# Kernel optimization log

Measured on AMD Instinct MI355X. Metric: run time of the kernel, lower is better.

Reference implementation:

```python
import jax, jax.numpy as jnp
import numpy as np

ITERATION = 3
NEG = -2.0**16 + 1.0  # mask fill value from the torch code


def setup_inputs() -> dict:
    key = jax.random.key(0)
    k1, k2, k3, k4 = jax.random.split(key, 4)
    B, L, D_in, D_out, K = 1024, 512, 64, 64, 8
    low_capsule = jax.random.normal(k1, (B, L, D_in), dtype=jnp.float32)
    B_init = jax.random.normal(k2, (1, K, L), dtype=jnp.float32)
    S = jax.random.normal(k3, (D_in, D_out), dtype=jnp.float32)
    seq_len = jax.random.randint(k4, (B, 1), 1, L + 1, dtype=jnp.int32)
    return {"low_capsule": low_capsule, "B_init": B_init, "S": S, "seq_len": seq_len}


def _squash(x):
    # torch code sums squared norm over dim=1 (the capsule/max_k dim), keepdim
    sq = jnp.sum(jnp.square(x), axis=1, keepdims=True)
    scale = sq / (1.0 + sq) / jnp.sqrt(sq + 1e-9)
    return scale * x


def reference(low_capsule, B_init, S, seq_len):
    # low_capsule: [B, L, D_in], B_init: [1, K, L], S: [D_in, D_out], seq_len: [B, 1]
    Bsz, L, _ = low_capsule.shape
    K = B_init.shape[1]
    # sequence mask: [B, K, L] (seq_len tiled over K)
    mask = jnp.arange(L, dtype=seq_len.dtype)[None, None, :] < seq_len[:, :, None]
    mask = jnp.broadcast_to(mask, (Bsz, K, L))
    # bilinear projection is loop-invariant; compute once
    low_new = jnp.einsum('bld,do->blo', low_capsule, S)  # [B, L, D_out]
    B_mat = B_init
    high = None
    for _ in range(ITERATION):
        logits = jnp.where(mask, B_mat, NEG)               # [B, K, L]
        W = jax.nn.softmax(logits, axis=-1)                # masked softmax
        high = _squash(jnp.einsum('bkl,blo->bko', W, low_new))  # [B, K, D_out]
        B_delta = jnp.sum(jnp.einsum('bko,blo->bkl', high, low_new),
                          axis=0, keepdims=True)           # [1, K, L]
        B_mat = B_mat + B_delta
    return high
```

## Files before the change

kernel.cpp:

```cpp
#include <hip/hip_runtime.h>

#define NEG_FILL (-65535.0f)
#define NSLOT 32

typedef __attribute__((ext_vector_type(8))) short  short8;
typedef __attribute__((ext_vector_type(4))) float  floatx4;

__device__ inline unsigned short f2bf(float f) {
    unsigned u = __float_as_uint(f);
    u += 0x7FFFu + ((u >> 16) & 1u);
    return (unsigned short)(u >> 16);
}
__device__ inline float bf2f(unsigned short h) {
    return __uint_as_float(((unsigned)h) << 16);
}
__device__ __forceinline__ short8 pack8(float4 a, float4 b) {
    short8 f;
    f[0] = (short)f2bf(a.x); f[1] = (short)f2bf(a.y);
    f[2] = (short)f2bf(a.z); f[3] = (short)f2bf(a.w);
    f[4] = (short)f2bf(b.x); f[5] = (short)f2bf(b.y);
    f[6] = (short)f2bf(b.z); f[7] = (short)f2bf(b.w);
    return f;
}

__global__ __launch_bounds__(256) void k_init(const float* __restrict__ Binit,
                                              float* __restrict__ B0,
                                              float* __restrict__ slots) {
    int i = blockIdx.x * 256 + threadIdx.x;
    slots[i] = 0.f;
    if (i < 4096) B0[i] = Binit[i];
}

__global__ __launch_bounds__(256) void k_bred(const float* __restrict__ Bcur,
                                              float* __restrict__ Bnext,
                                              float* __restrict__ slots) {
    int i = blockIdx.x * 256 + threadIdx.x;
    float s = Bcur[i];
    #pragma unroll
    for (int j = 0; j < NSLOT; ++j) {
        s += slots[j * 4096 + i];
        slots[j * 4096 + i] = 0.f;
    }
    Bnext[i] = s;
}

__device__ __forceinline__ void softmax_to_WsT(
    const float* __restrict__ Bc, int sl, int lane, int g,
    float (*WsT)[8]) {
    #pragma unroll
    for (int kk = 0; kk < 2; ++kk) {
        const int k = g + (kk << 2);
        float v[8];
        float mx = NEG_FILL;
        #pragma unroll
        for (int j = 0; j < 8; ++j) {
            int l = lane + (j << 6);
            v[j] = (l < sl) ? Bc[(k << 9) + l] : NEG_FILL;
            mx = fmaxf(mx, v[j]);
        }
        #pragma unroll
        for (int off = 32; off; off >>= 1) mx = fmaxf(mx, __shfl_xor(mx, off));
        float s = 0.f;
        #pragma unroll
        for (int j = 0; j < 8; ++j) { v[j] = expf(v[j] - mx); s += v[j]; }
        #pragma unroll
        for (int off = 32; off; off >>= 1) s += __shfl_xor(s, off);
        const float inv = 1.0f / s;
        #pragma unroll
        for (int j = 0; j < 8; ++j) WsT[lane + (j << 6)][k] = v[j] * inv;
    }
}

__global__ __launch_bounds__(256, 4) void k_lnT(
    const float* __restrict__ low,
    const float* __restrict__ S,
    const float* __restrict__ Bc,
    const int* __restrict__ seq_len,
    unsigned short* __restrict__ ln,
    float* __restrict__ hout)
{
    __shared__ __align__(16) float WsT[512][8];
    __shared__ __align__(16) float Tpart[4][8][64];
    __shared__ __align__(16) float Tred[8][64];

    const int t = threadIdx.x, lane = t & 63, g = t >> 6, b = blockIdx.x;
    const int m = lane & 15, q = lane >> 4;
    const int sl = seq_len[b];
    const float* lowb = low + ((size_t)b << 15);
    unsigned short* lnb = ln + ((size_t)b << 15);

    softmax_to_WsT(Bc, sl, lane, g, WsT);
    __syncthreads();

    short8 sfrag[4][2];
    #pragma unroll
    for (int nt = 0; nt < 4; ++nt)
        #pragma unroll
        for (int dh = 0; dh < 2; ++dh) {
            short8 f;
            #pragma unroll
            for (int j = 0; j < 8; ++j) {
                int d = dh * 32 + q * 8 + j;
                f[j] = (short)f2bf(S[(d << 6) + nt * 16 + m]);
            }
            sfrag[nt][dh] = f;
        }

    float Tp[8][4];
    #pragma unroll
    for (int k = 0; k < 8; ++k)
        #pragma unroll
        for (int nt = 0; nt < 4; ++nt) Tp[k][nt] = 0.f;

    for (int tt = 0; tt < 8; ++tt) {
        const int lt = (g << 7) + (tt << 4);
        short8 afrag[2];
        #pragma unroll
        for (int dh = 0; dh < 2; ++dh) {
            const float4* p =
                (const float4*)&lowb[((lt + m) << 6) + dh * 32 + q * 8];
            float4 x0 = p[0], x1 = p[1];
            short8 f;
            f[0] = (short)f2bf(x0.x); f[1] = (short)f2bf(x0.y);
            f[2] = (short)f2bf(x0.z); f[3] = (short)f2bf(x0.w);
            f[4] = (short)f2bf(x1.x); f[5] = (short)f2bf(x1.y);
            f[6] = (short)f2bf(x1.z); f[7] = (short)f2bf(x1.w);
            afrag[dh] = f;
        }
        float lnr[4][4];
        #pragma unroll
        for (int nt = 0; nt < 4; ++nt) {
            floatx4 acc = {0.f, 0.f, 0.f, 0.f};
            acc = __builtin_amdgcn_mfma_f32_16x16x32_bf16(afrag[0], sfrag[nt][0], acc, 0, 0, 0);
            acc = __builtin_amdgcn_mfma_f32_16x16x32_bf16(afrag[1], sfrag[nt][1], acc, 0, 0, 0);
            #pragma unroll
            for (int r = 0; r < 4; ++r) {
                unsigned short hb = f2bf(acc[r]);
                lnb[((size_t)(lt + (q << 2) + r) << 6) + nt * 16 + m] = hb;
                lnr[r][nt] = bf2f(hb);
            }
        }
        #pragma unroll
        for (int r = 0; r < 4; ++r) {
            const int l = lt + (q << 2) + r;
            const float4 wa = *(const float4*)&WsT[l][0];
            const float4 wb = *(const float4*)&WsT[l][4];
            #pragma unroll
            for (int nt = 0; nt < 4; ++nt) {
                const float x = lnr[r][nt];
                Tp[0][nt] = fmaf(wa.x, x, Tp[0][nt]);
                Tp[1][nt] = fmaf(wa.y, x, Tp[1][nt]);
                Tp[2][nt] = fmaf(wa.z, x, Tp[2][nt]);
                Tp[3][nt] = fmaf(wa.w, x, Tp[3][nt]);
                Tp[4][nt] = fmaf(wb.x, x, Tp[4][nt]);
                Tp[5][nt] = fmaf(wb.y, x, Tp[5][nt]);
                Tp[6][nt] = fmaf(wb.z, x, Tp[6][nt]);
                Tp[7][nt] = fmaf(wb.w, x, Tp[7][nt]);
            }
        }
    }
    #pragma unroll
    for (int k = 0; k < 8; ++k)
        #pragma unroll
        for (int nt = 0; nt < 4; ++nt) {
            float v = Tp[k][nt];
            v += __shfl_xor(v, 16);
            v += __shfl_xor(v, 32);
            Tp[k][nt] = v;
        }
    #pragma unroll
    for (int k = 0; k < 8; ++k) Tpart[g][k][lane] = Tp[k][q];
    __syncthreads();

    #pragma unroll
    for (int idx = t; idx < 512; idx += 256) {
        float s = (&Tpart[0][0][0])[idx] + (&Tpart[1][0][0])[idx]
                + (&Tpart[2][0][0])[idx] + (&Tpart[3][0][0])[idx];
        (&Tred[0][0])[idx] = s;
    }
    __syncthreads();

    float sq = 0.f;
    #pragma unroll
    for (int k = 0; k < 8; ++k) { float x = Tred[k][lane]; sq = fmaf(x, x, sq); }
    const float scale = sq / (1.0f + sq) / sqrtf(sq + 1e-9f);
    hout[((size_t)b << 9) + (g << 6) + lane]       = scale * Tred[g][lane];
    hout[((size_t)b << 9) + ((g + 4) << 6) + lane] = scale * Tred[g + 4][lane];
}

__global__ __launch_bounds__(256, 4) void k_T(
    const unsigned short* __restrict__ ln,
    const float* __restrict__ Bc,
    const int* __restrict__ seq_len,
    float* __restrict__ hout)
{
    __shared__ __align__(16) float WsT[512][8];
    __shared__ __align__(16) float Tpart[4][8][64];
    __shared__ __align__(16) float Tred[8][64];

    const int t = threadIdx.x, lane = t & 63, g = t >> 6, b = blockIdx.x;
    const int m = lane & 15, q = lane >> 4;
    const int sl = seq_len[b];
    const unsigned short* lnb = ln + ((size_t)b << 15);

    softmax_to_WsT(Bc, sl, lane, g, WsT);
    __syncthreads();

    floatx4 Tacc[8];
    #pragma unroll
    for (int k = 0; k < 8; ++k) Tacc[k] = (floatx4){0.f, 0.f, 0.f, 0.f};
    const int l0 = g << 7;
    const int rem = sl - l0;
    int nact = (rem <= 0) ? 0 : ((rem + 31) >> 5);
    if (nact > 4) nact = 4;

    for (int ii = 0; ii < nact; ++ii) {
        uint2 u[8];
        #pragma unroll
        for (int j = 0; j < 8; ++j) {
            const int l = l0 + (ii << 5) + (j << 2) + q;
            u[j] = *(const uint2*)&lnb[(l << 6) + (m << 2)];
        }
        #pragma unroll
        for (int j = 0; j < 8; ++j) {
            const int l = l0 + (ii << 5) + (j << 2) + q;
            const float x0 = __uint_as_float(u[j].x << 16);
            const float x1 = __uint_as_float(u[j].x & 0xFFFF0000u);
            const float x2 = __uint_as_float(u[j].y << 16);
            const float x3 = __uint_as_float(u[j].y & 0xFFFF0000u);
            const float4 wa = *(const float4*)&WsT[l][0];
            const float4 wb = *(const float4*)&WsT[l][4];
#define TROW(K, WV)                                          \
            Tacc[K][0] = fmaf(WV, x0, Tacc[K][0]);           \
            Tacc[K][1] = fmaf(WV, x1, Tacc[K][1]);           \
            Tacc[K][2] = fmaf(WV, x2, Tacc[K][2]);           \
            Tacc[K][3] = fmaf(WV, x3, Tacc[K][3]);
            TROW(0, wa.x) TROW(1, wa.y) TROW(2, wa.z) TROW(3, wa.w)
            TROW(4, wb.x) TROW(5, wb.y) TROW(6, wb.z) TROW(7, wb.w)
#undef TROW
        }
    }
    #pragma unroll
    for (int k = 0; k < 8; ++k)
        #pragma unroll
        for (int j = 0; j < 4; ++j) {
            float v = Tacc[k][j];
            v += __shfl_xor(v, 16);
            v += __shfl_xor(v, 32);
            Tacc[k][j] = v;
        }
    if (q == 0) {
        #pragma unroll
        for (int k = 0; k < 8; ++k)
            *(float4*)&Tpart[g][k][m << 2] =
                make_float4(Tacc[k][0], Tacc[k][1], Tacc[k][2], Tacc[k][3]);
    }
    __syncthreads();

    #pragma unroll
    for (int idx = t; idx < 512; idx += 256) {
        float s = (&Tpart[0][0][0])[idx] + (&Tpart[1][0][0])[idx]
                + (&Tpart[2][0][0])[idx] + (&Tpart[3][0][0])[idx];
        (&Tred[0][0])[idx] = s;
    }
    __syncthreads();

    float sq = 0.f;
    #pragma unroll
    for (int k = 0; k < 8; ++k) { float x = Tred[k][lane]; sq = fmaf(x, x, sq); }
    const float scale = sq / (1.0f + sq) / sqrtf(sq + 1e-9f);
    hout[((size_t)b << 9) + (g << 6) + lane]       = scale * Tred[g][lane];
    hout[((size_t)b << 9) + ((g + 4) << 6) + lane] = scale * Tred[g + 4][lane];
}

__global__ __launch_bounds__(256, 8) void k_delta(
    const unsigned short* __restrict__ ln,
    const float* __restrict__ hout,
    float* __restrict__ slots)
{
    const int t = threadIdx.x, lane = t & 63, g = t >> 6;
    const int bb = blockIdx.x, b = bb >> 1, half = bb & 1;
    const int m = lane & 15, q = lane >> 4;
    const unsigned short* lnb = ln + ((size_t)b << 15);
    const float* hb = hout + ((size_t)b << 9);
    float* slot = slots + ((size_t)(b & (NSLOT - 1)) << 12);

    short8 afragH[2];
    #pragma unroll
    for (int oh = 0; oh < 2; ++oh) {
        short8 f = {0, 0, 0, 0, 0, 0, 0, 0};
        if (m < 8) {
            const float4* p = (const float4*)&hb[(m << 6) + oh * 32 + q * 8];
            f = pack8(p[0], p[1]);
        }
        afragH[oh] = f;
    }
    const int lbase = (half << 8) + (g << 6);
    #pragma unroll
    for (int pp = 0; pp < 2; ++pp) {
        short8 bf[2][2];
        #pragma unroll
        for (int u = 0; u < 2; ++u) {
            const int lt = lbase + (((pp << 1) + u) << 4);
            const unsigned short* p = &lnb[((lt + m) << 6) + q * 8];
            bf[u][0] = *(const short8*)p;
            bf[u][1] = *(const short8*)(p + 32);
        }
        #pragma unroll
        for (int u = 0; u < 2; ++u) {
            const int lt = lbase + (((pp << 1) + u) << 4);
            floatx4 acc = {0.f, 0.f, 0.f, 0.f};
            acc = __builtin_amdgcn_mfma_f32_16x16x32_bf16(afragH[0], bf[u][0], acc, 0, 0, 0);
            acc = __builtin_amdgcn_mfma_f32_16x16x32_bf16(afragH[1], bf[u][1], acc, 0, 0, 0);
            if (q < 2) {
                #pragma unroll
                for (int r = 0; r < 4; ++r)
                    atomicAdd(&slot[((q << 2) + r) * 512 + lt + m], acc[r]);
            }
        }
    }
}

__global__ __launch_bounds__(256) void k_copy4k(const float* __restrict__ src,
                                                float* __restrict__ dst) {
    int i = blockIdx.x * 256 + threadIdx.x;
    dst[i] = src[i];
}

__global__ __launch_bounds__(256, 4) void k_route(
    const float* __restrict__ low, const float* __restrict__ S,
    const float* __restrict__ Bcur, float* __restrict__ Bnext,
    const int* __restrict__ seq_len, float* __restrict__ out, int last)
{
    __shared__ float smemA[64 * 65];
    __shared__ float Spad[64][65];
    __shared__ float GT[64][8];
    __shared__ float Tred[8][64];
    float* WsT = smemA;
    float (*Tpart)[8][64] = (float (*)[8][64])smemA;
    float (*tile)[65]     = (float (*)[65])smemA;

    const int t = threadIdx.x, o = t & 63, g = t >> 6, b = blockIdx.x;
    const int sl = seq_len[b];
    const float* lowb = low + ((size_t)b << 15);

    #pragma unroll
    for (int i = 0; i < 16; ++i) {
        int idx = t + (i << 8);
        Spad[idx >> 6][idx & 63] = S[idx];
    }
    #pragma unroll
    for (int kk = 0; kk < 2; ++kk) {
        const int k = g + (kk << 2);
        float v[8];
        float mx = NEG_FILL;
        #pragma unroll
        for (int j = 0; j < 8; ++j) {
            int l = o + (j << 6);
            v[j] = (l < sl) ? Bcur[(k << 9) + l] : NEG_FILL;
            mx = fmaxf(mx, v[j]);
        }
        #pragma unroll
        for (int off = 32; off; off >>= 1) mx = fmaxf(mx, __shfl_xor(mx, off));
        float s = 0.f;
        #pragma unroll
        for (int j = 0; j < 8; ++j) { v[j] = expf(v[j] - mx); s += v[j]; }
        #pragma unroll
        for (int off = 32; off; off >>= 1) s += __shfl_xor(s, off);
        const float inv = 1.0f / s;
        #pragma unroll
        for (int j = 0; j < 8; ++j) WsT[((o + (j << 6)) << 3) + k] = v[j] * inv;
    }
    __syncthreads();

    float Ta[8];
    #pragma unroll
    for (int k = 0; k < 8; ++k) Ta[k] = 0.f;
    {
        const int l0 = g << 7;
        #pragma unroll 4
        for (int i = 0; i < 128; ++i) {
            const int l = l0 + i;
            const float x = lowb[(l << 6) + o];
            const float4 wa = *(const float4*)&WsT[(l << 3)];
            const float4 wb = *(const float4*)&WsT[(l << 3) + 4];
            Ta[0] = fmaf(wa.x, x, Ta[0]); Ta[1] = fmaf(wa.y, x, Ta[1]);
            Ta[2] = fmaf(wa.z, x, Ta[2]); Ta[3] = fmaf(wa.w, x, Ta[3]);
            Ta[4] = fmaf(wb.x, x, Ta[4]); Ta[5] = fmaf(wb.y, x, Ta[5]);
            Ta[6] = fmaf(wb.z, x, Ta[6]); Ta[7] = fmaf(wb.w, x, Ta[7]);
        }
    }
    __syncthreads();
    #pragma unroll
    for (int k = 0; k < 8; ++k) Tpart[g][k][o] = Ta[k];
    __syncthreads();

    float h0 = 0.f, h1 = 0.f;
    #pragma unroll
    for (int gg = 0; gg < 4; ++gg) { h0 += Tpart[gg][g][o]; h1 += Tpart[gg][g + 4][o]; }
    Tred[g][o] = h0; Tred[g + 4][o] = h1;
    __syncthreads();

    float hp0 = 0.f, hp1 = 0.f;
    #pragma unroll
    for (int d = 0; d < 64; ++d) {
        const float sv = Spad[d][o];
        hp0 = fmaf(Tred[g][d], sv, hp0);
        hp1 = fmaf(Tred[g + 4][d], sv, hp1);
    }
    __syncthreads();
    Tred[g][o] = hp0; Tred[g + 4][o] = hp1;
    __syncthreads();

    float sq = 0.f;
    #pragma unroll
    for (int k = 0; k < 8; ++k) { float x = Tred[k][o]; sq = fmaf(x, x, sq); }
    const float scale = sq / (1.0f + sq) / sqrtf(sq + 1e-9f);
    const float hf0 = scale * hp0;
    const float hf1 = scale * hp1;

    if (last) {
        out[(((size_t)b * 8 + g)     << 6) + o] = hf0;
        out[(((size_t)b * 8 + g + 4) << 6) + o] = hf1;
        return;
    }
    __syncthreads();
    Tred[g][o] = hf0; Tred[g + 4][o] = hf1;
    __syncthreads();

    float g0 = 0.f, g1 = 0.f;
    #pragma unroll
    for (int oo = 0; oo < 64; ++oo) {
        const float sv = Spad[o][oo];
        g0 = fmaf(Tred[g][oo], sv, g0);
        g1 = fmaf(Tred[g + 4][oo], sv, g1);
    }
    GT[o][g] = g0; GT[o][g + 4] = g1;
    __syncthreads();

    for (int c = 0; c < 8; ++c) {
        const int lc = c << 6;
        #pragma unroll
        for (int r = 0; r < 16; ++r) {
            const int lr = (g << 4) + r;
            tile[lr][o] = lowb[((lc + lr) << 6) + o];
        }
        __syncthreads();
        float a0 = 0.f, a1 = 0.f;
        #pragma unroll
        for (int d = 0; d < 64; ++d) {
            const float x = tile[o][d];
            a0 = fmaf(GT[d][g], x, a0);
            a1 = fmaf(GT[d][g + 4], x, a1);
        }
        atomicAdd(&Bnext[(g << 9) + lc + o], a0);
        atomicAdd(&Bnext[((g + 4) << 9) + lc + o], a1);
        __syncthreads();
    }
}

extern "C" void kernel_launch(void* const* d_in, const int* in_sizes, int n_in,
                              void* d_out, int out_size, void* d_ws, size_t ws_size,
                              hipStream_t stream) {
    const float* low   = (const float*)d_in[0];
    const float* Binit = (const float*)d_in[1];
    const float* S     = (const float*)d_in[2];
    const int*   seq   = (const int*)d_in[3];
    float* outp = (float*)d_out;

    const size_t LN_BYTES   = (size_t)1024 * 512 * 64 * 2;
    const size_t SLOT_BYTES = (size_t)NSLOT * 4096 * sizeof(float);
    const size_t NEED = LN_BYTES + SLOT_BYTES + 2 * 4096 * sizeof(float);

    if (ws_size >= NEED) {
        unsigned short* lnw = (unsigned short*)d_ws;
        float* slots = (float*)((char*)d_ws + LN_BYTES);
        float* B0 = slots + (size_t)NSLOT * 4096;
        float* B1 = B0 + 4096;

        k_init<<<(NSLOT * 4096) / 256, 256, 0, stream>>>(Binit, B0, slots);

        k_lnT<<<1024, 256, 0, stream>>>(low, S, B0, seq, lnw, outp);
        k_delta<<<2048, 256, 0, stream>>>(lnw, outp, slots);
        k_bred<<<16, 256, 0, stream>>>(B0, B1, slots);

        k_T<<<1024, 256, 0, stream>>>(lnw, B1, seq, outp);
        k_delta<<<2048, 256, 0, stream>>>(lnw, outp, slots);
        k_bred<<<16, 256, 0, stream>>>(B1, B0, slots);

        k_T<<<1024, 256, 0, stream>>>(lnw, B0, seq, outp);
    } else {
        float* B0 = (float*)d_ws;
        float* B1 = B0 + 4096;
        k_copy4k<<<16, 256, 0, stream>>>(Binit, B0);
        k_copy4k<<<16, 256, 0, stream>>>(B0, B1);
        k_route<<<1024, 256, 0, stream>>>(low, S, B0, B1, seq, outp, 0);
        k_copy4k<<<16, 256, 0, stream>>>(B1, B0);
        k_route<<<1024, 256, 0, stream>>>(low, S, B1, B0, seq, outp, 0);
        k_route<<<1024, 256, 0, stream>>>(low, S, B0, nullptr, seq, outp, 1);
    }
}
```

Before: 282.9 us.

## Split k_T across two blocks per batch over output-dimension halves

The routing-weighted sum kernel now launches two blocks per batch, each covering 32 of the 64 output features, with launch bounds raised to 7 blocks per CU. This halves per-thread accumulators and shared-memory footprint to raise occupancy and the number of blocks in flight. The cost is that each block recomputes the masked softmax into shared memory, and the per-lane global loads shrink to 4 bytes.

```diff
diff --git a/kernel.cpp b/kernel.cpp
--- a/kernel.cpp
+++ b/kernel.cpp
@@ -188,53 +188,50 @@
     hout[((size_t)b << 9) + ((g + 4) << 6) + lane] = scale * Tred[g + 4][lane];
 }
 
-__global__ __launch_bounds__(256, 4) void k_T(
+__global__ __launch_bounds__(256, 7) void k_T(
     const unsigned short* __restrict__ ln,
     const float* __restrict__ Bc,
     const int* __restrict__ seq_len,
     float* __restrict__ hout)
 {
     __shared__ __align__(16) float WsT[512][8];
-    __shared__ __align__(16) float Tpart[4][8][64];
-    __shared__ __align__(16) float Tred[8][64];
-
-    const int t = threadIdx.x, lane = t & 63, g = t >> 6, b = blockIdx.x;
+    __shared__ __align__(16) float Tpart[4][8][32];
+    __shared__ __align__(16) float Tred[8][32];
+
+    const int t = threadIdx.x, lane = t & 63, g = t >> 6;
+    const int bb = blockIdx.x, b = bb >> 1, oh = bb & 1;
     const int m = lane & 15, q = lane >> 4;
     const int sl = seq_len[b];
-    const unsigned short* lnb = ln + ((size_t)b << 15);
+    const unsigned short* lnb = ln + ((size_t)b << 15) + (oh << 5);
 
     softmax_to_WsT(Bc, sl, lane, g, WsT);
     __syncthreads();
 
-    floatx4 Tacc[8];
-    #pragma unroll
-    for (int k = 0; k < 8; ++k) Tacc[k] = (floatx4){0.f, 0.f, 0.f, 0.f};
+    float Tacc[8][2];
+    #pragma unroll
+    for (int k = 0; k < 8; ++k) { Tacc[k][0] = 0.f; Tacc[k][1] = 0.f; }
     const int l0 = g << 7;
     const int rem = sl - l0;
     int nact = (rem <= 0) ? 0 : ((rem + 31) >> 5);
     if (nact > 4) nact = 4;
 
     for (int ii = 0; ii < nact; ++ii) {
-        uint2 u[8];
+        unsigned u[8];
         #pragma unroll
         for (int j = 0; j < 8; ++j) {
             const int l = l0 + (ii << 5) + (j << 2) + q;
-            u[j] = *(const uint2*)&lnb[(l << 6) + (m << 2)];
+            u[j] = *(const unsigned*)&lnb[(l << 6) + (m << 1)];
         }
         #pragma unroll
         for (int j = 0; j < 8; ++j) {
             const int l = l0 + (ii << 5) + (j << 2) + q;
-            const float x0 = __uint_as_float(u[j].x << 16);
-            const float x1 = __uint_as_float(u[j].x & 0xFFFF0000u);
-            const float x2 = __uint_as_float(u[j].y << 16);
-            const float x3 = __uint_as_float(u[j].y & 0xFFFF0000u);
+            const float x0 = __uint_as_float(u[j] << 16);
+            const float x1 = __uint_as_float(u[j] & 0xFFFF0000u);
             const float4 wa = *(const float4*)&WsT[l][0];
             const float4 wb = *(const float4*)&WsT[l][4];
 #define TROW(K, WV)                                          \
             Tacc[K][0] = fmaf(WV, x0, Tacc[K][0]);           \
-            Tacc[K][1] = fmaf(WV, x1, Tacc[K][1]);           \
-            Tacc[K][2] = fmaf(WV, x2, Tacc[K][2]);           \
-            Tacc[K][3] = fmaf(WV, x3, Tacc[K][3]);
+            Tacc[K][1] = fmaf(WV, x1, Tacc[K][1]);
             TROW(0, wa.x) TROW(1, wa.y) TROW(2, wa.z) TROW(3, wa.w)
             TROW(4, wb.x) TROW(5, wb.y) TROW(6, wb.z) TROW(7, wb.w)
 #undef TROW
@@ -243,7 +240,7 @@
     #pragma unroll
     for (int k = 0; k < 8; ++k)
         #pragma unroll
-        for (int j = 0; j < 4; ++j) {
+        for (int j = 0; j < 2; ++j) {
             float v = Tacc[k][j];
             v += __shfl_xor(v, 16);
             v += __shfl_xor(v, 32);
@@ -252,25 +249,24 @@
     if (q == 0) {
         #pragma unroll
         for (int k = 0; k < 8; ++k)
-            *(float4*)&Tpart[g][k][m << 2] =
-                make_float4(Tacc[k][0], Tacc[k][1], Tacc[k][2], Tacc[k][3]);
-    }
-    __syncthreads();
-
-    #pragma unroll
-    for (int idx = t; idx < 512; idx += 256) {
-        float s = (&Tpart[0][0][0])[idx] + (&Tpart[1][0][0])[idx]
-                + (&Tpart[2][0][0])[idx] + (&Tpart[3][0][0])[idx];
-        (&Tred[0][0])[idx] = s;
-    }
-    __syncthreads();
-
+            *(float2*)&Tpart[g][k][m << 1] =
+                make_float2(Tacc[k][0], Tacc[k][1]);
+    }
+    __syncthreads();
+
+    {
+        float s = (&Tpart[0][0][0])[t] + (&Tpart[1][0][0])[t]
+                + (&Tpart[2][0][0])[t] + (&Tpart[3][0][0])[t];
+        (&Tred[0][0])[t] = s;
+    }
+    __syncthreads();
+
+    const int k = t >> 5, o = t & 31;
     float sq = 0.f;
     #pragma unroll
-    for (int k = 0; k < 8; ++k) { float x = Tred[k][lane]; sq = fmaf(x, x, sq); }
+    for (int kk = 0; kk < 8; ++kk) { float x = Tred[kk][o]; sq = fmaf(x, x, sq); }
     const float scale = sq / (1.0f + sq) / sqrtf(sq + 1e-9f);
-    hout[((size_t)b << 9) + (g << 6) + lane]       = scale * Tred[g][lane];
-    hout[((size_t)b << 9) + ((g + 4) << 6) + lane] = scale * Tred[g + 4][lane];
+    hout[((size_t)b << 9) + (k << 6) + (oh << 5) + o] = scale * Tred[k][o];
 }
 
 __global__ __launch_bounds__(256, 8) void k_delta(
@@ -484,11 +480,11 @@
         k_delta<<<2048, 256, 0, stream>>>(lnw, outp, slots);
         k_bred<<<16, 256, 0, stream>>>(B0, B1, slots);
 
-        k_T<<<1024, 256, 0, stream>>>(lnw, B1, seq, outp);
+        k_T<<<2048, 256, 0, stream>>>(lnw, B1, seq, outp);
         k_delta<<<2048, 256, 0, stream>>>(lnw, outp, slots);
         k_bred<<<16, 256, 0, stream>>>(B1, B0, slots);
 
-        k_T<<<1024, 256, 0, stream>>>(lnw, B0, seq, outp);
+        k_T<<<2048, 256, 0, stream>>>(lnw, B0, seq, outp);
     } else {
         float* B0 = (float*)d_ws;
         float* B1 = B0 + 4096;
```

Result: slower. 291.2 us (+2.9%).
